# Performance work log

Measured on AMD Instinct MI355X. Metric: run time of the kernel, lower is better.

## Reference

```python
import jax, jax.numpy as jnp
import numpy as np

H = 512
B = 128
S = 512


def setup_inputs() -> dict:
    key = jax.random.key(0)
    ks = jax.random.split(key, 12)
    s = 1.0 / np.sqrt(H)
    return {
        "input": jax.random.normal(ks[0], (B, H), jnp.float32),
        "h": jax.random.normal(ks[1], (B, H), jnp.float32),
        "c": jax.random.normal(ks[2], (B, H), jnp.float32),
        "enc_outputs": jax.random.normal(ks[3], (B, S, H), jnp.float32),
        "mask": jnp.ones((B, S), jnp.float32),
        # attention params
        "W1": jax.random.uniform(ks[4], (H, H), jnp.float32, -s, s),
        "W2": jax.random.uniform(ks[5], (H, H), jnp.float32, -s, s),
        "b2": jax.random.uniform(ks[6], (H,), jnp.float32, -s, s),
        "V": jax.random.uniform(ks[7], (H, 1), jnp.float32, -s, s),
        # LSTMCell params (torch gate order: i, f, g, o)
        "W_ih": jax.random.uniform(ks[8], (4 * H, H), jnp.float32, -s, s),
        "W_hh": jax.random.uniform(ks[9], (4 * H, H), jnp.float32, -s, s),
        "b_ih": jax.random.uniform(ks[10], (4 * H,), jnp.float32, -s, s),
        "b_hh": jax.random.uniform(ks[11], (4 * H,), jnp.float32, -s, s),
    }


def _lstm_cell(x, h, c, W_ih, W_hh, b_ih, b_hh):
    gates = x @ W_ih.T + b_ih + h @ W_hh.T + b_hh  # [B, 4H]
    i, f, g, o = jnp.split(gates, 4, axis=1)
    i = jax.nn.sigmoid(i)
    f = jax.nn.sigmoid(f)
    g = jnp.tanh(g)
    o = jax.nn.sigmoid(o)
    c_new = f * c + i * g
    h_new = o * jnp.tanh(c_new)
    return h_new, c_new


def reference(input, h, c, enc_outputs, mask, W1, W2, b2, V, W_ih, W_hh, b_ih, b_hh):
    h_new, c_new = _lstm_cell(input, h, c, W_ih, W_hh, b_ih, b_hh)
    # Bahdanau additive attention
    w1e = jnp.einsum("bsh,oh->bso", enc_outputs, W1)          # [B,S,H]
    w2h = (h_new @ W2.T + b2)[:, None, :]                      # [B,1,H]
    u = jnp.tanh(w1e + w2h)                                    # [B,S,H]
    a = jnp.einsum("bsh,h->bs", u, V[:, 0])                    # [B,S]
    a = 10.0 * jnp.tanh(a)
    policy = jax.nn.softmax(a + jnp.log(mask), axis=1)         # [B,S]
    return policy, h_new, c_new
```

## Files before the change

### kernel.cpp

```cpp
#include <hip/hip_runtime.h>
#include <hip/hip_bf16.h>
#include <math.h>

typedef __bf16 bf16;
typedef __bf16 bf16x4 __attribute__((ext_vector_type(4)));
typedef __bf16 bf16x8 __attribute__((ext_vector_type(8)));
typedef float  f32x4  __attribute__((ext_vector_type(4)));

#define HD 512
#define NB 128
#define NS 512
#define MS (NB*NS)

__device__ __forceinline__ float sigmoidf_(float x){ return 1.0f/(1.0f+expf(-x)); }

__device__ __forceinline__ float fast_tanh(float x){
    float ax = fabsf(x);
    float e  = __expf(-2.0f*ax);
    float t  = (1.0f - e) * __builtin_amdgcn_rcpf(1.0f + e);
    return copysignf(t, x);
}

__global__ __launch_bounds__(256) void cvt_w1_frag(const float* __restrict__ W1, bf16* __restrict__ W1s){
    int wid = blockIdx.x*4 + (threadIdx.x>>6);
    int l   = threadIdx.x & 63;
    int fn = wid >> 4, ki = wid & 15;
    int row = fn*16 + (l & 15);
    int kk  = ki*32 + (l >> 4)*8;
    const f32x4* gp = (const f32x4*)&W1[(size_t)row*512 + kk];
    f32x4 v0 = gp[0], v1 = gp[1];
    bf16x8 hv;
    #pragma unroll
    for (int j=0;j<4;++j){ hv[j]=(bf16)v0[j]; hv[4+j]=(bf16)v1[j]; }
    *(bf16x8*)&W1s[(size_t)((fn*16 + ki)*64 + l)*8] = hv;
}

__global__ __launch_bounds__(256) void gemm_split(
    const float* __restrict__ A1, const float* __restrict__ A2,
    const float* __restrict__ B1, const float* __restrict__ B2,
    const float* __restrict__ bias1, const float* __restrict__ bias2,
    float* __restrict__ C, int N, int Ksegs)
{
    __shared__ bf16 Ah[64][32], Al[64][32], Bh[64][32], Bl[64][32];
    int tid = threadIdx.x;
    int bm = blockIdx.x, bn = blockIdx.y;
    int w = tid>>6, l = tid&63;
    int wm = w>>1, wn = w&1;
    f32x4 acc[2][2] = {};
    int KT = Ksegs*512;
    for (int k0 = 0; k0 < KT; k0 += 32){
        const float* Ap = (k0 < 512) ? A1 : A2;
        const float* Bp = (k0 < 512) ? B1 : B2;
        int kk = k0 & 511;
        __syncthreads();
        #pragma unroll
        for (int q = 0; q < 2; ++q){
            int id  = q*256 + tid;
            int row = id >> 3, c4 = (id & 7)*4;
            f32x4 va = *(const f32x4*)&Ap[(size_t)(bm*64+row)*512 + kk + c4];
            f32x4 vb = *(const f32x4*)&Bp[(size_t)(bn*64+row)*512 + kk + c4];
            bf16x4 vah, val_, vbh, vbl;
            #pragma unroll
            for (int j=0;j<4;++j){
                bf16 ha = (bf16)va[j]; vah[j]=ha; val_[j]=(bf16)(va[j]-(float)ha);
                bf16 hb = (bf16)vb[j]; vbh[j]=hb; vbl[j]=(bf16)(vb[j]-(float)hb);
            }
            *(bf16x4*)&Ah[row][c4] = vah;  *(bf16x4*)&Al[row][c4] = val_;
            *(bf16x4*)&Bh[row][c4] = vbh;  *(bf16x4*)&Bl[row][c4] = vbl;
        }
        __syncthreads();
        int koff = (l>>4)*8;
        int ar = wm*32 + (l&15);
        int br = wn*32 + (l&15);
        bf16x8 ah[2], al[2], bh[2], bl[2];
        ah[0]=*(const bf16x8*)&Ah[ar][koff];    ah[1]=*(const bf16x8*)&Ah[ar+16][koff];
        al[0]=*(const bf16x8*)&Al[ar][koff];    al[1]=*(const bf16x8*)&Al[ar+16][koff];
        bh[0]=*(const bf16x8*)&Bh[br][koff];    bh[1]=*(const bf16x8*)&Bh[br+16][koff];
        bl[0]=*(const bf16x8*)&Bl[br][koff];    bl[1]=*(const bf16x8*)&Bl[br+16][koff];
        #pragma unroll
        for (int fm=0; fm<2; ++fm)
        #pragma unroll
        for (int fn=0; fn<2; ++fn){
            acc[fm][fn] = __builtin_amdgcn_mfma_f32_16x16x32_bf16(ah[fm], bh[fn], acc[fm][fn],0,0,0);
            acc[fm][fn] = __builtin_amdgcn_mfma_f32_16x16x32_bf16(ah[fm], bl[fn], acc[fm][fn],0,0,0);
            acc[fm][fn] = __builtin_amdgcn_mfma_f32_16x16x32_bf16(al[fm], bh[fn], acc[fm][fn],0,0,0);
        }
    }
    #pragma unroll
    for (int fm=0; fm<2; ++fm)
    #pragma unroll
    for (int fn=0; fn<2; ++fn){
        #pragma unroll
        for (int r=0; r<4; ++r){
            int m = bm*64 + wm*32 + fm*16 + ((l>>4)<<2) + r;
            int n = bn*64 + wn*32 + fn*16 + (l&15);
            float bias = 0.f;
            if (bias1) bias += bias1[m];
            if (bias2) bias += bias2[m];
            C[(size_t)m*N + n] = acc[fm][fn][r] + bias;
        }
    }
}

__global__ __launch_bounds__(256) void lstm_pointwise(
    const float* __restrict__ gates, const float* __restrict__ c_in,
    float* __restrict__ h_out, float* __restrict__ c_out)
{
    int t = blockIdx.x*256 + threadIdx.x;
    int b = t >> 9, hh = t & 511;
    float gi = gates[(size_t)(0*512+hh)*128 + b];
    float gf = gates[(size_t)(1*512+hh)*128 + b];
    float gg = gates[(size_t)(2*512+hh)*128 + b];
    float go = gates[(size_t)(3*512+hh)*128 + b];
    float i = sigmoidf_(gi), f = sigmoidf_(gf), g = tanhf(gg), o = sigmoidf_(go);
    float cn = f*c_in[t] + i*g;
    float hn = o*tanhf(cn);
    h_out[t] = hn;  c_out[t] = cn;
}

__global__ __launch_bounds__(512,4) void attn_main(
    const float* __restrict__ enc, const bf16* __restrict__ W1s,
    const float* __restrict__ w2h, const float* __restrict__ Vv,
    float* __restrict__ a_out)
{
    __shared__ bf16 Alds[64*512];
    __shared__ float w2h_s[512];
    __shared__ float V_s[512];
    __shared__ float red[64][8];
    int tid = threadIdx.x;
    int w = tid>>6, l = tid&63;
    int m0 = blockIdx.x * 64;
    int bidx = blockIdx.x >> 3;
    w2h_s[tid] = w2h[(size_t)tid*128 + bidx];
    V_s[tid]   = Vv[tid];

    const int lr = l & 15, lk = l >> 4;
    const bf16* Bbase = W1s + (size_t)w*32768 + (size_t)l*8;

    bf16x8 bA[4], bB[4];
    #pragma unroll
    for (int fn=0; fn<4; ++fn) bA[fn] = *(const bf16x8*)(Bbase + fn*8192);

    #pragma unroll
    for (int it = 0; it < 8; ++it){
        int c   = it*512 + tid;
        int row = c >> 6, s = c & 63;
        const f32x4* gp = (const f32x4*)&enc[(size_t)(m0+row)*512 + s*8];
        f32x4 v0 = gp[0], v1 = gp[1];
        bf16x8 hv;
        #pragma unroll
        for (int j=0;j<4;++j){ hv[j]=(bf16)v0[j]; hv[4+j]=(bf16)v1[j]; }
        int slot = s ^ (row & 15);
        *(bf16x8*)((char*)Alds + row*1024 + slot*16) = hv;
    }
    __syncthreads();

    f32x4 acc[4][4] = {};

    #pragma unroll
    for (int kp = 0; kp < 8; ++kp){
        int ki0 = 2*kp, ki1 = 2*kp+1;
        #pragma unroll
        for (int fn=0; fn<4; ++fn) bB[fn] = *(const bf16x8*)(Bbase + fn*8192 + ki1*512);
        {
            bf16x8 af[4];
            #pragma unroll
            for (int fm=0; fm<4; ++fm){
                int row = fm*16 + lr;
                int slot = (ki0*4 + lk) ^ (row & 15);
                af[fm] = *(const bf16x8*)((const char*)Alds + row*1024 + slot*16);
            }
            #pragma unroll
            for (int fm=0; fm<4; ++fm)
            #pragma unroll
            for (int fn=0; fn<4; ++fn)
                acc[fm][fn] = __builtin_amdgcn_mfma_f32_16x16x32_bf16(af[fm], bA[fn], acc[fm][fn],0,0,0);
        }
        if (kp < 7){
            #pragma unroll
            for (int fn=0; fn<4; ++fn) bA[fn] = *(const bf16x8*)(Bbase + fn*8192 + (ki0+2)*512);
        }
        {
            bf16x8 af[4];
            #pragma unroll
            for (int fm=0; fm<4; ++fm){
                int row = fm*16 + lr;
                int slot = (ki1*4 + lk) ^ (row & 15);
                af[fm] = *(const bf16x8*)((const char*)Alds + row*1024 + slot*16);
            }
            #pragma unroll
            for (int fm=0; fm<4; ++fm)
            #pragma unroll
            for (int fn=0; fn<4; ++fn)
                acc[fm][fn] = __builtin_amdgcn_mfma_f32_16x16x32_bf16(af[fm], bB[fn], acc[fm][fn],0,0,0);
        }
    }

    #pragma unroll
    for (int fm=0; fm<4; ++fm){
        float asum[4] = {0.f,0.f,0.f,0.f};
        #pragma unroll
        for (int fn=0; fn<4; ++fn){
            int o = w*64 + fn*16 + lr;
            float wv = w2h_s[o], vv = V_s[o];
            #pragma unroll
            for (int r=0;r<4;++r)
                asum[r] += fast_tanh(acc[fm][fn][r] + wv) * vv;
        }
        #pragma unroll
        for (int off=1; off<16; off<<=1){
            #pragma unroll
            for (int r=0;r<4;++r) asum[r] += __shfl_xor(asum[r], off, 64);
        }
        if (lr == 0){
            #pragma unroll
            for (int r=0;r<4;++r) red[fm*16 + lk*4 + r][w] = asum[r];
        }
    }
    __syncthreads();
    if (tid < 64){
        float a = 0.f;
        #pragma unroll
        for (int q=0;q<8;++q) a += red[tid][q];
        a_out[m0 + tid] = 10.0f * fast_tanh(a);
    }
}

__global__ __launch_bounds__(512) void softmax_k(
    const float* __restrict__ a10, const float* __restrict__ mask,
    float* __restrict__ out)
{
    int b = blockIdx.x, tid = threadIdx.x;
    __shared__ float sred[8];
    float v = a10[(size_t)b*512 + tid] + logf(mask[(size_t)b*512 + tid]);
    float m = v;
    #pragma unroll
    for (int off=1; off<64; off<<=1) m = fmaxf(m, __shfl_xor(m, off, 64));
    if ((tid&63)==0) sred[tid>>6] = m;
    __syncthreads();
    float mt = sred[0];
    #pragma unroll
    for (int i=1;i<8;++i) mt = fmaxf(mt, sred[i]);
    float e = expf(v - mt);
    float s = e;
    #pragma unroll
    for (int off=1; off<64; off<<=1) s += __shfl_xor(s, off, 64);
    __syncthreads();
    if ((tid&63)==0) sred[tid>>6] = s;
    __syncthreads();
    float st = 0.f;
    #pragma unroll
    for (int i=0;i<8;++i) st += sred[i];
    out[(size_t)b*512 + tid] = e / st;
}

extern "C" void kernel_launch(void* const* d_in, const int* in_sizes, int n_in,
                              void* d_out, int out_size, void* d_ws, size_t ws_size,
                              hipStream_t stream)
{
    const float* x    = (const float*)d_in[0];
    const float* h    = (const float*)d_in[1];
    const float* c    = (const float*)d_in[2];
    const float* enc  = (const float*)d_in[3];
    const float* mask = (const float*)d_in[4];
    const float* W1   = (const float*)d_in[5];
    const float* W2   = (const float*)d_in[6];
    const float* b2   = (const float*)d_in[7];
    const float* V    = (const float*)d_in[8];
    const float* Wih  = (const float*)d_in[9];
    const float* Whh  = (const float*)d_in[10];
    const float* bih  = (const float*)d_in[11];
    const float* bhh  = (const float*)d_in[12];

    float* out_policy = (float*)d_out;
    float* out_h = out_policy + MS;
    float* out_c = out_policy + 2*MS;

    float* ws_f  = (float*)d_ws;
    float* gates = ws_f;
    float* w2h   = ws_f + 262144;
    float* a10   = ws_f + 327680;
    bf16*  W1s   = (bf16*)(ws_f + 393216);

    cvt_w1_frag<<<128, 256, 0, stream>>>(W1, W1s);
    gemm_split<<<dim3(32,2), 256, 0, stream>>>(Wih, Whh, x, h, bih, bhh, gates, 128, 2);
    lstm_pointwise<<<256, 256, 0, stream>>>(gates, c, out_h, out_c);
    gemm_split<<<dim3(8,2), 256, 0, stream>>>(W2, nullptr, out_h, nullptr, b2, nullptr, w2h, 128, 1);
    attn_main<<<1024, 512, 0, stream>>>(enc, W1s, w2h, V, a10);
    softmax_k<<<128, 512, 0, stream>>>(a10, mask, out_policy);
}
```

Baseline: 112.1 us.

## Add producer warp pipelining to attention GEMM and split-K for small GEMMs

The attention kernel gains a dedicated producer wavefront that converts encoder chunks of 128 K-columns into a double-buffered LDS tile. The eight consumer wavefronts run MFMAs on one buffer while the next is being filled, replacing the single full-tile load followed by compute, and the W1 fragment layout is reordered to match the chunked K order. The LSTM and W2 GEMMs now use split-K over a z grid dimension and write transposed partial outputs, which the pointwise and attention kernels sum. This trades more workspace traffic and an extra wavefront per block (lower occupancy bound, 3 blocks) for overlap and more parallelism in the small GEMMs.

After: 96.24 us. 1.16x faster.

```diff
diff --git a/kernel.cpp b/kernel.cpp
--- a/kernel.cpp
+++ b/kernel.cpp
@@ -22,33 +22,34 @@
 }
 
 __global__ __launch_bounds__(256) void cvt_w1_frag(const float* __restrict__ W1, bf16* __restrict__ W1s){
-    int wid = blockIdx.x*4 + (threadIdx.x>>6);
-    int l   = threadIdx.x & 63;
-    int fn = wid >> 4, ki = wid & 15;
-    int row = fn*16 + (l & 15);
+    int F = blockIdx.x*4 + (threadIdx.x>>6);
+    int l = threadIdx.x & 63;
+    int fnl = F & 3, ki = (F>>2) & 15, w = F>>6;
+    int row = (w*4 + fnl)*16 + (l & 15);
     int kk  = ki*32 + (l >> 4)*8;
     const f32x4* gp = (const f32x4*)&W1[(size_t)row*512 + kk];
     f32x4 v0 = gp[0], v1 = gp[1];
     bf16x8 hv;
     #pragma unroll
     for (int j=0;j<4;++j){ hv[j]=(bf16)v0[j]; hv[4+j]=(bf16)v1[j]; }
-    *(bf16x8*)&W1s[(size_t)((fn*16 + ki)*64 + l)*8] = hv;
+    *(bf16x8*)&W1s[(size_t)F*512 + (size_t)l*8] = hv;
 }
 
 __global__ __launch_bounds__(256) void gemm_split(
     const float* __restrict__ A1, const float* __restrict__ A2,
     const float* __restrict__ B1, const float* __restrict__ B2,
     const float* __restrict__ bias1, const float* __restrict__ bias2,
-    float* __restrict__ C, int N, int Ksegs)
+    float* __restrict__ C, int N, int ksize, int ldct)
 {
     __shared__ bf16 Ah[64][32], Al[64][32], Bh[64][32], Bl[64][32];
     int tid = threadIdx.x;
-    int bm = blockIdx.x, bn = blockIdx.y;
+    int bm = blockIdx.x, bn = blockIdx.y, ks = blockIdx.z;
+    int kfrom = ks*ksize, kend = kfrom + ksize;
+    float* Cz = C + (size_t)ks * N * ldct;
     int w = tid>>6, l = tid&63;
     int wm = w>>1, wn = w&1;
     f32x4 acc[2][2] = {};
-    int KT = Ksegs*512;
-    for (int k0 = 0; k0 < KT; k0 += 32){
+    for (int k0 = kfrom; k0 < kend; k0 += 32){
         const float* Ap = (k0 < 512) ? A1 : A2;
         const float* Bp = (k0 < 512) ? B1 : B2;
         int kk = k0 & 511;
@@ -94,127 +95,139 @@
         for (int r=0; r<4; ++r){
             int m = bm*64 + wm*32 + fm*16 + ((l>>4)<<2) + r;
             int n = bn*64 + wn*32 + fn*16 + (l&15);
-            float bias = 0.f;
-            if (bias1) bias += bias1[m];
-            if (bias2) bias += bias2[m];
-            C[(size_t)m*N + n] = acc[fm][fn][r] + bias;
+            float v = acc[fm][fn][r];
+            if (ks == 0){
+                if (bias1) v += bias1[m];
+                if (bias2) v += bias2[m];
+            }
+            Cz[(size_t)n*ldct + m] = v;
         }
     }
 }
 
 __global__ __launch_bounds__(256) void lstm_pointwise(
-    const float* __restrict__ gates, const float* __restrict__ c_in,
+    const float* __restrict__ gatesT, const float* __restrict__ c_in,
     float* __restrict__ h_out, float* __restrict__ c_out)
 {
     int t = blockIdx.x*256 + threadIdx.x;
     int b = t >> 9, hh = t & 511;
-    float gi = gates[(size_t)(0*512+hh)*128 + b];
-    float gf = gates[(size_t)(1*512+hh)*128 + b];
-    float gg = gates[(size_t)(2*512+hh)*128 + b];
-    float go = gates[(size_t)(3*512+hh)*128 + b];
+    const float* gp = gatesT + (size_t)b*2048 + hh;
+    float gi=0.f, gf=0.f, gg=0.f, go=0.f;
+    #pragma unroll
+    for (int ks=0; ks<4; ++ks){
+        const float* p = gp + (size_t)ks*262144;
+        gi += p[0]; gf += p[512]; gg += p[1024]; go += p[1536];
+    }
     float i = sigmoidf_(gi), f = sigmoidf_(gf), g = tanhf(gg), o = sigmoidf_(go);
     float cn = f*c_in[t] + i*g;
     float hn = o*tanhf(cn);
     h_out[t] = hn;  c_out[t] = cn;
 }
 
-__global__ __launch_bounds__(512,4) void attn_main(
+__device__ __forceinline__ void pref_b(const bf16* base, bf16x8* dst){
+    #pragma unroll
+    for (int fnl=0; fnl<4; ++fnl) dst[fnl] = *(const bf16x8*)(base + fnl*512);
+}
+
+__device__ __forceinline__ void comp_par(const bf16* buf, int kil, int lr, int lk,
+                                         const bf16x8* b, f32x4 (&acc)[4][4]){
+    bf16x8 af[4];
+    #pragma unroll
+    for (int fm=0; fm<4; ++fm){
+        int row  = fm*16 + lr;
+        int slot = (kil*4 + lk) ^ (row & 15);
+        af[fm] = *(const bf16x8*)((const char*)buf + row*256 + slot*16);
+    }
+    #pragma unroll
+    for (int fm=0; fm<4; ++fm)
+    #pragma unroll
+    for (int fn=0; fn<4; ++fn)
+        acc[fm][fn] = __builtin_amdgcn_mfma_f32_16x16x32_bf16(af[fm], b[fn], acc[fm][fn],0,0,0);
+}
+
+__device__ __forceinline__ void produce_chunk(const float* ep, int kc, bf16* buf, int l){
+    #pragma unroll
+    for (int j=0; j<16; ++j){
+        int c = l + j*64;
+        int r = c >> 4, s = c & 15;
+        const float* p = ep + (size_t)r*512 + kc*128 + s*8;
+        f32x4 v0 = *(const f32x4*)p;
+        f32x4 v1 = *(const f32x4*)(p+4);
+        bf16x8 hv;
+        #pragma unroll
+        for (int jj=0;jj<4;++jj){ hv[jj]=(bf16)v0[jj]; hv[4+jj]=(bf16)v1[jj]; }
+        *(bf16x8*)((char*)buf + r*256 + ((s ^ (r & 15))*16)) = hv;
+    }
+}
+
+__global__ __launch_bounds__(576,3) void attn_main(
     const float* __restrict__ enc, const bf16* __restrict__ W1s,
-    const float* __restrict__ w2h, const float* __restrict__ Vv,
+    const float* __restrict__ w2hp, const float* __restrict__ Vv,
     float* __restrict__ a_out)
 {
-    __shared__ bf16 Alds[64*512];
+    __shared__ bf16 Alds[2][64*128];
     __shared__ float w2h_s[512];
     __shared__ float V_s[512];
     __shared__ float red[64][8];
-    int tid = threadIdx.x;
-    int w = tid>>6, l = tid&63;
-    int m0 = blockIdx.x * 64;
-    int bidx = blockIdx.x >> 3;
-    w2h_s[tid] = w2h[(size_t)tid*128 + bidx];
-    V_s[tid]   = Vv[tid];
-
+    const int tid = threadIdx.x, w = tid>>6, l = tid&63;
     const int lr = l & 15, lk = l >> 4;
-    const bf16* Bbase = W1s + (size_t)w*32768 + (size_t)l*8;
-
-    bf16x8 bA[4], bB[4];
-    #pragma unroll
-    for (int fn=0; fn<4; ++fn) bA[fn] = *(const bf16x8*)(Bbase + fn*8192);
-
-    #pragma unroll
-    for (int it = 0; it < 8; ++it){
-        int c   = it*512 + tid;
-        int row = c >> 6, s = c & 63;
-        const f32x4* gp = (const f32x4*)&enc[(size_t)(m0+row)*512 + s*8];
-        f32x4 v0 = gp[0], v1 = gp[1];
-        bf16x8 hv;
-        #pragma unroll
-        for (int j=0;j<4;++j){ hv[j]=(bf16)v0[j]; hv[4+j]=(bf16)v1[j]; }
-        int slot = s ^ (row & 15);
-        *(bf16x8*)((char*)Alds + row*1024 + slot*16) = hv;
-    }
-    __syncthreads();
-
-    f32x4 acc[4][4] = {};
-
-    #pragma unroll
-    for (int kp = 0; kp < 8; ++kp){
-        int ki0 = 2*kp, ki1 = 2*kp+1;
-        #pragma unroll
-        for (int fn=0; fn<4; ++fn) bB[fn] = *(const bf16x8*)(Bbase + fn*8192 + ki1*512);
-        {
-            bf16x8 af[4];
+    const int m0 = blockIdx.x * 64;
+    const int bidx = blockIdx.x >> 3;
+    if (tid < 512){
+        w2h_s[tid] = w2hp[(size_t)bidx*512 + tid] + w2hp[(size_t)65536 + bidx*512 + tid];
+        V_s[tid]   = Vv[tid];
+    }
+
+    if (w == 8){
+        const float* ep = enc + (size_t)m0*512;
+        produce_chunk(ep, 0, Alds[0], l);
+        __syncthreads();
+        produce_chunk(ep, 1, Alds[1], l);
+        __syncthreads();
+        produce_chunk(ep, 2, Alds[0], l);
+        __syncthreads();
+        produce_chunk(ep, 3, Alds[1], l);
+        __syncthreads();
+        __syncthreads();
+    } else {
+        const bf16* Bbase = W1s + (size_t)w*32768 + (size_t)l*8;
+        bf16x8 bA[4], bB[4];
+        pref_b(Bbase, bA);
+        f32x4 acc[4][4] = {};
+        __syncthreads();
+        #pragma unroll
+        for (int kc=0; kc<4; ++kc){
+            const bf16* bufc = Alds[kc&1];
+            pref_b(Bbase + (kc*4+1)*2048, bB);
+            comp_par(bufc, 0, lr, lk, bA, acc);
+            pref_b(Bbase + (kc*4+2)*2048, bA);
+            comp_par(bufc, 1, lr, lk, bB, acc);
+            pref_b(Bbase + (kc*4+3)*2048, bB);
+            comp_par(bufc, 2, lr, lk, bA, acc);
+            if (kc < 3) pref_b(Bbase + (kc*4+4)*2048, bA);
+            comp_par(bufc, 3, lr, lk, bB, acc);
+            __syncthreads();
+        }
+        #pragma unroll
+        for (int fm=0; fm<4; ++fm){
+            float asum[4] = {0.f,0.f,0.f,0.f};
             #pragma unroll
-            for (int fm=0; fm<4; ++fm){
-                int row = fm*16 + lr;
-                int slot = (ki0*4 + lk) ^ (row & 15);
-                af[fm] = *(const bf16x8*)((const char*)Alds + row*1024 + slot*16);
+            for (int fn=0; fn<4; ++fn){
+                int o = w*64 + fn*16 + lr;
+                float wv = w2h_s[o], vv = V_s[o];
+                #pragma unroll
+                for (int r=0;r<4;++r)
+                    asum[r] += fast_tanh(acc[fm][fn][r] + wv) * vv;
             }
             #pragma unroll
-            for (int fm=0; fm<4; ++fm)
-            #pragma unroll
-            for (int fn=0; fn<4; ++fn)
-                acc[fm][fn] = __builtin_amdgcn_mfma_f32_16x16x32_bf16(af[fm], bA[fn], acc[fm][fn],0,0,0);
-        }
-        if (kp < 7){
-            #pragma unroll
-            for (int fn=0; fn<4; ++fn) bA[fn] = *(const bf16x8*)(Bbase + fn*8192 + (ki0+2)*512);
-        }
-        {
-            bf16x8 af[4];
-            #pragma unroll
-            for (int fm=0; fm<4; ++fm){
-                int row = fm*16 + lr;
-                int slot = (ki1*4 + lk) ^ (row & 15);
-                af[fm] = *(const bf16x8*)((const char*)Alds + row*1024 + slot*16);
-            }
-            #pragma unroll
-            for (int fm=0; fm<4; ++fm)
-            #pragma unroll
-            for (int fn=0; fn<4; ++fn)
-                acc[fm][fn] = __builtin_amdgcn_mfma_f32_16x16x32_bf16(af[fm], bB[fn], acc[fm][fn],0,0,0);
-        }
-    }
-
-    #pragma unroll
-    for (int fm=0; fm<4; ++fm){
-        float asum[4] = {0.f,0.f,0.f,0.f};
-        #pragma unroll
-        for (int fn=0; fn<4; ++fn){
-            int o = w*64 + fn*16 + lr;
-            float wv = w2h_s[o], vv = V_s[o];
-            #pragma unroll
-            for (int r=0;r<4;++r)
-                asum[r] += fast_tanh(acc[fm][fn][r] + wv) * vv;
-        }
-        #pragma unroll
-        for (int off=1; off<16; off<<=1){
-            #pragma unroll
-            for (int r=0;r<4;++r) asum[r] += __shfl_xor(asum[r], off, 64);
-        }
-        if (lr == 0){
-            #pragma unroll
-            for (int r=0;r<4;++r) red[fm*16 + lk*4 + r][w] = asum[r];
+            for (int off=1; off<16; off<<=1){
+                #pragma unroll
+                for (int r=0;r<4;++r) asum[r] += __shfl_xor(asum[r], off, 64);
+            }
+            if (lr == 0){
+                #pragma unroll
+                for (int r=0;r<4;++r) red[fm*16 + lk*4 + r][w] = asum[r];
+            }
         }
     }
     __syncthreads();
@@ -276,16 +289,16 @@
     float* out_h = out_policy + MS;
     float* out_c = out_policy + 2*MS;
 
-    float* ws_f  = (float*)d_ws;
-    float* gates = ws_f;
-    float* w2h   = ws_f + 262144;
-    float* a10   = ws_f + 327680;
-    bf16*  W1s   = (bf16*)(ws_f + 393216);
+    float* ws_f   = (float*)d_ws;
+    float* gatesT = ws_f;
+    float* w2hp   = ws_f + 1048576;
+    float* a10    = ws_f + 1179648;
+    bf16*  W1s    = (bf16*)(ws_f + 1245184);
 
     cvt_w1_frag<<<128, 256, 0, stream>>>(W1, W1s);
-    gemm_split<<<dim3(32,2), 256, 0, stream>>>(Wih, Whh, x, h, bih, bhh, gates, 128, 2);
-    lstm_pointwise<<<256, 256, 0, stream>>>(gates, c, out_h, out_c);
-    gemm_split<<<dim3(8,2), 256, 0, stream>>>(W2, nullptr, out_h, nullptr, b2, nullptr, w2h, 128, 1);
-    attn_main<<<1024, 512, 0, stream>>>(enc, W1s, w2h, V, a10);
+    gemm_split<<<dim3(32,2,4), 256, 0, stream>>>(Wih, Whh, x, h, bih, bhh, gatesT, 128, 256, 2048);
+    lstm_pointwise<<<256, 256, 0, stream>>>(gatesT, c, out_h, out_c);
+    gemm_split<<<dim3(8,2,2), 256, 0, stream>>>(W2, nullptr, out_h, nullptr, b2, nullptr, w2hp, 128, 256, 512);
+    attn_main<<<1024, 576, 0, stream>>>(enc, W1s, w2hp, V, a10);
     softmax_k<<<128, 512, 0, stream>>>(a10, mask, out_policy);
 }
```
